# Performance work log

Hardware: AMD Instinct MI355X
Metric: run time of the kernel (lower is better)

Reference implementation:

```python
import jax, jax.numpy as jnp
import numpy as np

DIM = 1024
H = 16
D = DIM // H  # 64
M = 64
TAU = 0.1


def setup_inputs() -> dict:
    key = jax.random.key(0)
    ks = jax.random.split(key, 12)
    s = 1.0 / np.sqrt(DIM)
    inp = {
        "x": jax.random.normal(ks[0], (4, 2048, DIM), dtype=jnp.float32),
        "W_q": jax.random.uniform(ks[1], (DIM, DIM), jnp.float32, -s, s),
        "b_q": jax.random.uniform(ks[2], (DIM,), jnp.float32, -s, s),
        "W_k": jax.random.uniform(ks[3], (DIM, DIM), jnp.float32, -s, s),
        "b_k": jax.random.uniform(ks[4], (DIM,), jnp.float32, -s, s),
        "W_v": jax.random.uniform(ks[5], (DIM, DIM), jnp.float32, -s, s),
        "b_v": jax.random.uniform(ks[6], (DIM,), jnp.float32, -s, s),
        "W_alpha": jax.random.uniform(ks[7], (H * M, DIM), jnp.float32, -s, s),
        "b_alpha": jax.random.uniform(ks[8], (H * M,), jnp.float32, -s, s),
        "W_o": jax.random.uniform(ks[9], (DIM, DIM), jnp.float32, -s, s),
        "b_o": jax.random.uniform(ks[10], (DIM,), jnp.float32, -s, s),
    }
    return inp


def reference(x, W_q, b_q, W_k, b_k, W_v, b_v, W_alpha, b_alpha, W_o, b_o):
    B, S, _ = x.shape
    silu = jax.nn.silu
    # projections [B,S,H,D]
    q = silu(x @ W_q.T + b_q).reshape(B, S, H, D)
    k = silu(x @ W_k.T + b_k).reshape(B, S, H, D)
    v = silu(x @ W_v.T + b_v).reshape(B, S, H, D)
    alpha = jax.nn.sigmoid(x @ W_alpha.T + b_alpha) ** (1.0 / TAU)
    alpha = alpha.reshape(B, S, H, M)

    # time-major for scan: [S, B, H, ...]
    qT = jnp.moveaxis(q, 1, 0)
    kT = jnp.moveaxis(k, 1, 0)
    vT = jnp.moveaxis(v, 1, 0)
    aT = jnp.moveaxis(alpha, 1, 0)

    Ke0 = jnp.zeros((B, H, M, D), dtype=x.dtype)
    Ve0 = jnp.zeros((B, H, M, D), dtype=x.dtype)

    def step(carry, inputs):
        Ke, Ve = carry
        q_t, k_t, v_t, a_t = inputs  # [B,H,D], [B,H,D], [B,H,D], [B,H,M]
        a = a_t[..., None]  # [B,H,M,1]
        Ke = a * Ke + (1.0 - a) * k_t[:, :, None, :]
        Ve = a * Ve + (1.0 - a) * v_t[:, :, None, :]
        energy = jnp.einsum("bhmd,bhd->bhm", Ke, q_t)
        attn = jax.nn.softmax(energy, axis=-1)
        o_t = jnp.einsum("bhm,bhmd->bhd", attn, Ve)
        return (Ke, Ve), o_t

    _, oT = jax.lax.scan(step, (Ke0, Ve0), (qT, kT, vT, aT))  # [S,B,H,D]
    o = jnp.moveaxis(oT, 0, 1).reshape(B, S, H * D)
    return o @ W_o.T + b_o
```

## Files before the change

kernel.cpp:

```cpp
#include <hip/hip_runtime.h>

#define S_LEN 2048
#define KDIM 1024
#define EMIT 64
#define WARM 16

typedef __attribute__((ext_vector_type(4))) float f32x4;
typedef __attribute__((ext_vector_type(8))) _Float16 f16x8;
typedef __attribute__((ext_vector_type(4))) _Float16 f16x4;
typedef __attribute__((ext_vector_type(2))) _Float16 f16x2;

union U8 { f16x8 v; f16x2 p[4]; };

__device__ inline f16x2 bcast2(_Float16 x) { f16x2 r; r[0] = x; r[1] = x; return r; }

#if __has_builtin(__builtin_amdgcn_fdot2)
__device__ inline float fdot2(f16x2 a, f16x2 b, float c) { return __builtin_amdgcn_fdot2(a, b, c, false); }
#else
__device__ inline float fdot2(f16x2 a, f16x2 b, float c) {
    return c + (float)a[0] * (float)b[0] + (float)a[1] * (float)b[1];
}
#endif

__device__ inline void async16(const void* g, void* l) {
    typedef unsigned int __attribute__((address_space(1)))* gp_t;
    typedef unsigned int __attribute__((address_space(3)))* lp_t;
    __builtin_amdgcn_global_load_lds((gp_t)g, (lp_t)l, 16, 0, 0);
}

__global__ void cvt_f16(const float* __restrict__ s, _Float16* __restrict__ d, int n4) {
    int i = blockIdx.x * 256 + threadIdx.x;
    int st = gridDim.x * 256;
    for (; i < n4; i += st) {
        f32x4 v = ((const f32x4*)s)[i];
        f16x4 o;
        o[0] = (_Float16)v[0]; o[1] = (_Float16)v[1];
        o[2] = (_Float16)v[2]; o[3] = (_Float16)v[3];
        ((f16x4*)d)[i] = o;
    }
}

__global__ void cvt_w5(const float* __restrict__ w0, const float* __restrict__ w1,
                       const float* __restrict__ w2, const float* __restrict__ w3,
                       const float* __restrict__ w4,
                       _Float16* __restrict__ dcat, _Float16* __restrict__ dwo) {
    const int seg = blockIdx.y;
    const float* s = seg == 0 ? w0 : seg == 1 ? w1 : seg == 2 ? w2 : seg == 3 ? w3 : w4;
    _Float16* d = (seg < 4) ? (dcat + (size_t)seg * 1048576) : dwo;
    const int n4 = 1024 * 1024 / 4;
    int i = blockIdx.x * 256 + threadIdx.x;
    const int st = gridDim.x * 256;
    for (; i < n4; i += st) {
        f32x4 v = ((const f32x4*)s)[i];
        f16x4 o;
        o[0] = (_Float16)v[0]; o[1] = (_Float16)v[1];
        o[2] = (_Float16)v[2]; o[3] = (_Float16)v[3];
        ((f16x4*)d)[i] = o;
    }
}

template<int EPI>
__global__ __launch_bounds__(256)
void gemm_bt(const _Float16* __restrict__ A, const _Float16* __restrict__ Bw,
             const float* __restrict__ bias0, const float* __restrict__ bias1,
             const float* __restrict__ bias2, const float* __restrict__ bias3,
             _Float16* __restrict__ outS, float* __restrict__ outF)
{
    __shared__ _Float16 ldsA[128 * 32];
    __shared__ _Float16 ldsB[128 * 32];
    const int tid = threadIdx.x;
    const int l = tid & 63, wid = tid >> 6;
    const int bm = blockIdx.x, bn = blockIdx.y;
    const int wr = wid >> 1, wc = wid & 1;

    f32x4 acc[4][4];
#pragma unroll
    for (int i = 0; i < 4; i++)
#pragma unroll
        for (int j = 0; j < 4; j++) { f32x4 z = {0.f, 0.f, 0.f, 0.f}; acc[i][j] = z; }

    const int rsub = wid * 16 + (l >> 2);
    const int ck = (l & 3) * 8;
    const _Float16* ga = A + (size_t)(bm * 128 + rsub) * KDIM + ck;
    const _Float16* gb = Bw + (size_t)(bn * 128 + rsub) * KDIM + ck;
    char* la = (char*)ldsA + wid * 1024;
    char* lb = (char*)ldsB + wid * 1024;

    for (int kt = 0; kt < KDIM / 32; ++kt) {
        __syncthreads();
        const _Float16* gak = ga + kt * 32;
        const _Float16* gbk = gb + kt * 32;
        async16(gak, la);
        async16(gak + (size_t)64 * KDIM, la + 4096);
        async16(gbk, lb);
        async16(gbk + (size_t)64 * KDIM, lb + 4096);
        __syncthreads();

        f16x8 af[4], bfr[4];
        const int rowb = l & 15;
        const int kb = (l >> 4) * 16;
#pragma unroll
        for (int mi = 0; mi < 4; mi++)
            af[mi] = *(const f16x8*)((const char*)ldsA + (wr * 64 + mi * 16 + rowb) * 64 + kb);
#pragma unroll
        for (int ni = 0; ni < 4; ni++)
            bfr[ni] = *(const f16x8*)((const char*)ldsB + (wc * 64 + ni * 16 + rowb) * 64 + kb);
#pragma unroll
        for (int mi = 0; mi < 4; mi++)
#pragma unroll
            for (int ni = 0; ni < 4; ni++)
                acc[mi][ni] = __builtin_amdgcn_mfma_f32_16x16x32_f16(af[mi], bfr[ni], acc[mi][ni], 0, 0, 0);
    }

    if (EPI == 0) {
        const int proj = bn >> 3;
        const int colbase = (bn & 7) * 128;
        const float* bias = proj == 0 ? bias0 : proj == 1 ? bias1 : proj == 2 ? bias2 : bias3;
        const int part = proj == 0 ? 2 : proj == 1 ? 0 : proj == 2 ? 1 : 3;
#pragma unroll
        for (int mi = 0; mi < 4; mi++) {
#pragma unroll
            for (int ni = 0; ni < 4; ni++) {
                const int c = colbase + wc * 64 + ni * 16 + (l & 15);
                const int h = c >> 6, jj = c & 63;
                const float bv = bias[c];
#pragma unroll
                for (int i = 0; i < 4; i++) {
                    const int gr = bm * 128 + wr * 64 + mi * 16 + ((l >> 4) * 4 + i);
                    const int b = gr >> 11, t = gr & 2047;
                    float z = acc[mi][ni][i] + bv;
                    float sg = 1.f / (1.f + __expf(-z));
                    float val;
                    if (proj < 3) val = z * sg;
                    else { float p2 = sg * sg, p4 = p2 * p2, p8 = p4 * p4; val = p8 * p2; }
                    outS[(((size_t)(b * 16 + h) * S_LEN + t) * 4 + part) * 64 + jj] = (_Float16)val;
                }
            }
        }
    } else {
#pragma unroll
        for (int mi = 0; mi < 4; mi++)
#pragma unroll
            for (int ni = 0; ni < 4; ni++) {
                const int gc = bn * 128 + wc * 64 + ni * 16 + (l & 15);
                const float bv = bias0[gc];
#pragma unroll
                for (int i = 0; i < 4; i++) {
                    const int gr = bm * 128 + wr * 64 + mi * 16 + ((l >> 4) * 4 + i);
                    outF[(size_t)gr * 1024 + gc] = acc[mi][ni][i] + bv;
                }
            }
    }
}

__global__ __launch_bounds__(256)
void scan_fused(const _Float16* __restrict__ strm, _Float16* __restrict__ oh)
{
    __shared__ float eb[2][256];
    __shared__ float obuf[2][256];
    __shared__ _Float16 at16[64];
    const int tid = threadIdx.x, l = tid & 63, w = tid >> 6;
    const int bh = blockIdx.x, c = blockIdx.y;
    const int b = bh >> 4, h = bh & 15;
    const int warm = (c == 0) ? 0 : WARM;
    const int start = c * EMIT - warm;
    const int nsteps = warm + EMIT;
    const f16x2 one2 = bcast2((_Float16)1.f);

    f16x2 ke2[8], ve2[8];
#pragma unroll
    for (int j = 0; j < 8; ++j) { ke2[j] = bcast2((_Float16)0.f); ve2[j] = bcast2((_Float16)0.f); }

    const _Float16* rp = strm + (size_t)(bh * S_LEN + start) * 256;
    _Float16* op = oh + (size_t)b * S_LEN * 1024 + h * 64 + l;

    U8 kA, kB, aA, aB, qA, qB;
    kA.v = *(const f16x8*)(rp + w * 16);
    kB.v = *(const f16x8*)(rp + w * 16 + 8);
    aA.v = *(const f16x8*)(rp + 192 + w * 16);
    aB.v = *(const f16x8*)(rp + 192 + w * 16 + 8);
    _Float16 a_l = rp[192 + l];
    _Float16 v_l = rp[64 + l];

    for (int s = 0; s < warm; ++s) {
        const f16x2 am2 = bcast2(a_l);
        const f16x2 om2 = one2 - am2;
        const f16x2 vd2 = bcast2(v_l);
#pragma unroll
        for (int j = 0; j < 4; ++j) {
            ke2[j]     = am2 * ke2[j]     + om2 * kA.p[j];
            ke2[4 + j] = am2 * ke2[4 + j] + om2 * kB.p[j];
            ve2[j]     = aA.p[j] * (ve2[j]     - vd2) + vd2;
            ve2[4 + j] = aB.p[j] * (ve2[4 + j] - vd2) + vd2;
        }
        const _Float16* r2 = rp + (size_t)(s + 1) * 256;
        kA.v = *(const f16x8*)(r2 + w * 16);
        kB.v = *(const f16x8*)(r2 + w * 16 + 8);
        aA.v = *(const f16x8*)(r2 + 192 + w * 16);
        aB.v = *(const f16x8*)(r2 + 192 + w * 16 + 8);
        a_l = r2[192 + l];
        v_l = r2[64 + l];
    }

    {
        const _Float16* r2 = rp + (size_t)warm * 256;
        qA.v = *(const f16x8*)(r2 + 128 + w * 16);
        qB.v = *(const f16x8*)(r2 + 128 + w * 16 + 8);
    }

    for (int s = warm; s < nsteps; ++s) {
        const int ep = (s - warm) & 1;
        const f16x2 am2 = bcast2(a_l);
        const f16x2 om2 = one2 - am2;
        const f16x2 vd2 = bcast2(v_l);
        float e0 = 0.f, e1 = 0.f;
#pragma unroll
        for (int j = 0; j < 4; ++j) {
            ke2[j]     = am2 * ke2[j]     + om2 * kA.p[j];
            ke2[4 + j] = am2 * ke2[4 + j] + om2 * kB.p[j];
            e0 = fdot2(ke2[j],     qA.p[j], e0);
            e1 = fdot2(ke2[4 + j], qB.p[j], e1);
            ve2[j]     = aA.p[j] * (ve2[j]     - vd2) + vd2;
            ve2[4 + j] = aB.p[j] * (ve2[4 + j] - vd2) + vd2;
        }
        eb[ep][tid] = e0 + e1;
        __syncthreads();

        if (s + 1 < nsteps) {
            const _Float16* r2 = rp + (size_t)(s + 1) * 256;
            kA.v = *(const f16x8*)(r2 + w * 16);
            kB.v = *(const f16x8*)(r2 + w * 16 + 8);
            aA.v = *(const f16x8*)(r2 + 192 + w * 16);
            aB.v = *(const f16x8*)(r2 + 192 + w * 16 + 8);
            qA.v = *(const f16x8*)(r2 + 128 + w * 16);
            qB.v = *(const f16x8*)(r2 + 128 + w * 16 + 8);
            a_l = r2[192 + l];
            v_l = r2[64 + l];
        }
        if (w == 0 && s > warm) {
            const int q = 1 - ep;
            const float o4 = obuf[q][l] + obuf[q][64 + l] + obuf[q][128 + l] + obuf[q][192 + l];
            op[(size_t)(start + s - 1) * 1024] = (_Float16)o4;
        }
        const float E = eb[ep][l] + eb[ep][64 + l] + eb[ep][128 + l] + eb[ep][192 + l];
        const float pr = __expf(E);
        float ps = pr;
#pragma unroll
        for (int d2 = 1; d2 < 64; d2 <<= 1) ps += __shfl_xor(ps, d2);
        const float at = pr / ps;
        if ((l >> 4) == w) at16[l] = (_Float16)at;
        U8 A0, A1;
        A0.v = *(const f16x8*)&at16[w * 16];
        A1.v = *(const f16x8*)&at16[w * 16 + 8];
        float o0 = 0.f, o1 = 0.f;
#pragma unroll
        for (int j = 0; j < 4; ++j) {
            o0 = fdot2(A0.p[j], ve2[j],     o0);
            o1 = fdot2(A1.p[j], ve2[4 + j], o1);
        }
        obuf[ep][tid] = o0 + o1;
    }
    __syncthreads();
    if (w == 0) {
        const int ep = (EMIT - 1) & 1;
        const float o4 = obuf[ep][l] + obuf[ep][64 + l] + obuf[ep][128 + l] + obuf[ep][192 + l];
        op[(size_t)(start + nsteps - 1) * 1024] = (_Float16)o4;
    }
}

extern "C" void kernel_launch(void* const* d_in, const int* in_sizes, int n_in,
                              void* d_out, int out_size, void* d_ws, size_t ws_size,
                              hipStream_t stream)
{
    const float* x  = (const float*)d_in[0];
    const float* Wq = (const float*)d_in[1];
    const float* bq = (const float*)d_in[2];
    const float* Wk = (const float*)d_in[3];
    const float* bk = (const float*)d_in[4];
    const float* Wv = (const float*)d_in[5];
    const float* bv = (const float*)d_in[6];
    const float* Wa = (const float*)d_in[7];
    const float* ba = (const float*)d_in[8];
    const float* Wo = (const float*)d_in[9];
    const float* bo = (const float*)d_in[10];
    float* out = (float*)d_out;

    char* w = (char*)d_ws;
    _Float16* xh   = (_Float16*)(w);
    _Float16* wcat = (_Float16*)(w + (16ull << 20));
    _Float16* woh  = (_Float16*)(w + (24ull << 20));
    _Float16* strm = (_Float16*)(w + (26ull << 20));
    _Float16* oh   = (_Float16*)(w + (90ull << 20));

    cvt_f16<<<512, 256, 0, stream>>>(x, xh, 8192 * 1024 / 4);
    cvt_w5<<<dim3(256, 5), 256, 0, stream>>>(Wq, Wk, Wv, Wa, Wo, wcat, woh);

    gemm_bt<0><<<dim3(64, 32), 256, 0, stream>>>(xh, wcat, bq, bk, bv, ba, strm, nullptr);

    scan_fused<<<dim3(64, 32), 256, 0, stream>>>(strm, oh);

    gemm_bt<1><<<dim3(64, 8), 256, 0, stream>>>(oh, woh, bo, nullptr, nullptr, nullptr, nullptr, out);
}
```

Baseline: 370.6 us.

## Process two scan steps per barrier and remap GEMM block order for XCDs

The scan loop now advances two timesteps per iteration. It computes both energy vectors before a single __syncthreads, runs both softmaxes and output dots together, and stores the intermediate V state so step one's output uses the right value. This halves the per-step barrier and LDS round-trip latency on the serial recurrence, at the cost of more registers and double-buffered loads. The GEMM also remaps linear block ids so consecutive tiles land on the same XCD (stride of 8), which should improve L2 locality. The remap hardcodes bm = newid & 63, which assumes a grid of 64 row tiles.

```diff
diff --git a/kernel.cpp b/kernel.cpp
--- a/kernel.cpp
+++ b/kernel.cpp
@@ -70,7 +70,11 @@
     __shared__ _Float16 ldsB[128 * 32];
     const int tid = threadIdx.x;
     const int l = tid & 63, wid = tid >> 6;
-    const int bm = blockIdx.x, bn = blockIdx.y;
+    const int fid = blockIdx.x + ((int)gridDim.x) * blockIdx.y;
+    const int per = ((int)(gridDim.x * gridDim.y)) >> 3;
+    const int newid = (fid & 7) * per + (fid >> 3);
+    const int bm = newid & 63;
+    const int bn = newid >> 6;
     const int wr = wid >> 1, wc = wid & 1;
 
     f32x4 acc[4][4];
@@ -157,8 +161,8 @@
 void scan_fused(const _Float16* __restrict__ strm, _Float16* __restrict__ oh)
 {
     __shared__ float eb[2][256];
-    __shared__ float obuf[2][256];
-    __shared__ _Float16 at16[64];
+    __shared__ float obuf[2][2][256];
+    __shared__ _Float16 at16[2][64];
     const int tid = threadIdx.x, l = tid & 63, w = tid >> 6;
     const int bh = blockIdx.x, c = blockIdx.y;
     const int b = bh >> 4, h = bh & 15;
@@ -167,104 +171,168 @@
     const int nsteps = warm + EMIT;
     const f16x2 one2 = bcast2((_Float16)1.f);
 
-    f16x2 ke2[8], ve2[8];
+    f16x2 ke2[8], ve2[8], vsn[8];
 #pragma unroll
     for (int j = 0; j < 8; ++j) { ke2[j] = bcast2((_Float16)0.f); ve2[j] = bcast2((_Float16)0.f); }
 
     const _Float16* rp = strm + (size_t)(bh * S_LEN + start) * 256;
     _Float16* op = oh + (size_t)b * S_LEN * 1024 + h * 64 + l;
 
-    U8 kA, kB, aA, aB, qA, qB;
-    kA.v = *(const f16x8*)(rp + w * 16);
-    kB.v = *(const f16x8*)(rp + w * 16 + 8);
-    aA.v = *(const f16x8*)(rp + 192 + w * 16);
-    aB.v = *(const f16x8*)(rp + 192 + w * 16 + 8);
-    _Float16 a_l = rp[192 + l];
-    _Float16 v_l = rp[64 + l];
+    U8 kA0, kB0, aA0, aB0, qA0, qB0, kA1, kB1, aA1, aB1, qA1, qB1;
+    kA0.v = *(const f16x8*)(rp + w * 16);
+    kB0.v = *(const f16x8*)(rp + w * 16 + 8);
+    aA0.v = *(const f16x8*)(rp + 192 + w * 16);
+    aB0.v = *(const f16x8*)(rp + 192 + w * 16 + 8);
+    _Float16 a0 = rp[192 + l];
+    _Float16 v0 = rp[64 + l];
+    _Float16 a1, v1;
 
     for (int s = 0; s < warm; ++s) {
-        const f16x2 am2 = bcast2(a_l);
+        const f16x2 am2 = bcast2(a0);
         const f16x2 om2 = one2 - am2;
-        const f16x2 vd2 = bcast2(v_l);
+        const f16x2 vd2 = bcast2(v0);
 #pragma unroll
         for (int j = 0; j < 4; ++j) {
-            ke2[j]     = am2 * ke2[j]     + om2 * kA.p[j];
-            ke2[4 + j] = am2 * ke2[4 + j] + om2 * kB.p[j];
-            ve2[j]     = aA.p[j] * (ve2[j]     - vd2) + vd2;
-            ve2[4 + j] = aB.p[j] * (ve2[4 + j] - vd2) + vd2;
+            ke2[j]     = am2 * ke2[j]     + om2 * kA0.p[j];
+            ke2[4 + j] = am2 * ke2[4 + j] + om2 * kB0.p[j];
+            ve2[j]     = aA0.p[j] * (ve2[j]     - vd2) + vd2;
+            ve2[4 + j] = aB0.p[j] * (ve2[4 + j] - vd2) + vd2;
         }
         const _Float16* r2 = rp + (size_t)(s + 1) * 256;
-        kA.v = *(const f16x8*)(r2 + w * 16);
-        kB.v = *(const f16x8*)(r2 + w * 16 + 8);
-        aA.v = *(const f16x8*)(r2 + 192 + w * 16);
-        aB.v = *(const f16x8*)(r2 + 192 + w * 16 + 8);
-        a_l = r2[192 + l];
-        v_l = r2[64 + l];
+        kA0.v = *(const f16x8*)(r2 + w * 16);
+        kB0.v = *(const f16x8*)(r2 + w * 16 + 8);
+        aA0.v = *(const f16x8*)(r2 + 192 + w * 16);
+        aB0.v = *(const f16x8*)(r2 + 192 + w * 16 + 8);
+        a0 = r2[192 + l];
+        v0 = r2[64 + l];
     }
 
     {
-        const _Float16* r2 = rp + (size_t)warm * 256;
-        qA.v = *(const f16x8*)(r2 + 128 + w * 16);
-        qB.v = *(const f16x8*)(r2 + 128 + w * 16 + 8);
-    }
-
-    for (int s = warm; s < nsteps; ++s) {
-        const int ep = (s - warm) & 1;
-        const f16x2 am2 = bcast2(a_l);
-        const f16x2 om2 = one2 - am2;
-        const f16x2 vd2 = bcast2(v_l);
-        float e0 = 0.f, e1 = 0.f;
+        const _Float16* r0 = rp + (size_t)warm * 256;
+        qA0.v = *(const f16x8*)(r0 + 128 + w * 16);
+        qB0.v = *(const f16x8*)(r0 + 128 + w * 16 + 8);
+        const _Float16* r1 = r0 + 256;
+        kA1.v = *(const f16x8*)(r1 + w * 16);
+        kB1.v = *(const f16x8*)(r1 + w * 16 + 8);
+        qA1.v = *(const f16x8*)(r1 + 128 + w * 16);
+        qB1.v = *(const f16x8*)(r1 + 128 + w * 16 + 8);
+        aA1.v = *(const f16x8*)(r1 + 192 + w * 16);
+        aB1.v = *(const f16x8*)(r1 + 192 + w * 16 + 8);
+        a1 = r1[192 + l];
+        v1 = r1[64 + l];
+    }
+
+    for (int s = warm; s < nsteps; s += 2) {
+        const int pp = ((s - warm) >> 1) & 1;
+        {
+            const f16x2 am2 = bcast2(a0);
+            const f16x2 om2 = one2 - am2;
+            const f16x2 vd2 = bcast2(v0);
+            float e0 = 0.f, e1 = 0.f;
+#pragma unroll
+            for (int j = 0; j < 4; ++j) {
+                ke2[j]     = am2 * ke2[j]     + om2 * kA0.p[j];
+                ke2[4 + j] = am2 * ke2[4 + j] + om2 * kB0.p[j];
+                e0 = fdot2(ke2[j],     qA0.p[j], e0);
+                e1 = fdot2(ke2[4 + j], qB0.p[j], e1);
+                ve2[j]     = aA0.p[j] * (ve2[j]     - vd2) + vd2;
+                ve2[4 + j] = aB0.p[j] * (ve2[4 + j] - vd2) + vd2;
+            }
+#pragma unroll
+            for (int j = 0; j < 8; ++j) vsn[j] = ve2[j];
+            eb[0][tid] = e0 + e1;
+        }
+        {
+            const f16x2 am2 = bcast2(a1);
+            const f16x2 om2 = one2 - am2;
+            const f16x2 vd2 = bcast2(v1);
+            float e0 = 0.f, e1 = 0.f;
+#pragma unroll
+            for (int j = 0; j < 4; ++j) {
+                ke2[j]     = am2 * ke2[j]     + om2 * kA1.p[j];
+                ke2[4 + j] = am2 * ke2[4 + j] + om2 * kB1.p[j];
+                e0 = fdot2(ke2[j],     qA1.p[j], e0);
+                e1 = fdot2(ke2[4 + j], qB1.p[j], e1);
+                ve2[j]     = aA1.p[j] * (ve2[j]     - vd2) + vd2;
+                ve2[4 + j] = aB1.p[j] * (ve2[4 + j] - vd2) + vd2;
+            }
+            eb[1][tid] = e0 + e1;
+        }
+        __syncthreads();
+
+        if (s + 2 < nsteps) {
+            const _Float16* r0 = rp + (size_t)(s + 2) * 256;
+            kA0.v = *(const f16x8*)(r0 + w * 16);
+            kB0.v = *(const f16x8*)(r0 + w * 16 + 8);
+            qA0.v = *(const f16x8*)(r0 + 128 + w * 16);
+            qB0.v = *(const f16x8*)(r0 + 128 + w * 16 + 8);
+            aA0.v = *(const f16x8*)(r0 + 192 + w * 16);
+            aB0.v = *(const f16x8*)(r0 + 192 + w * 16 + 8);
+            a0 = r0[192 + l];
+            v0 = r0[64 + l];
+            const _Float16* r1 = r0 + 256;
+            kA1.v = *(const f16x8*)(r1 + w * 16);
+            kB1.v = *(const f16x8*)(r1 + w * 16 + 8);
+            qA1.v = *(const f16x8*)(r1 + 128 + w * 16);
+            qB1.v = *(const f16x8*)(r1 + 128 + w * 16 + 8);
+            aA1.v = *(const f16x8*)(r1 + 192 + w * 16);
+            aB1.v = *(const f16x8*)(r1 + 192 + w * 16 + 8);
+            a1 = r1[192 + l];
+            v1 = r1[64 + l];
+        }
+        if (s > warm) {
+            const int qq = 1 - pp;
+            if (w == 0) {
+                const float o4 = obuf[qq][0][l] + obuf[qq][0][64 + l] +
+                                 obuf[qq][0][128 + l] + obuf[qq][0][192 + l];
+                op[(size_t)(start + s - 2) * 1024] = (_Float16)o4;
+            } else if (w == 1) {
+                const float o4 = obuf[qq][1][l] + obuf[qq][1][64 + l] +
+                                 obuf[qq][1][128 + l] + obuf[qq][1][192 + l];
+                op[(size_t)(start + s - 1) * 1024] = (_Float16)o4;
+            }
+        }
+        const float E0 = eb[0][l] + eb[0][64 + l] + eb[0][128 + l] + eb[0][192 + l];
+        const float E1 = eb[1][l] + eb[1][64 + l] + eb[1][128 + l] + eb[1][192 + l];
+        const float p0 = __expf(E0);
+        const float p1 = __expf(E1);
+        float s0 = p0, s1 = p1;
+#pragma unroll
+        for (int d2 = 1; d2 < 64; d2 <<= 1) {
+            s0 += __shfl_xor(s0, d2);
+            s1 += __shfl_xor(s1, d2);
+        }
+        const float at0 = p0 / s0;
+        const float at1 = p1 / s1;
+        if ((l >> 4) == w) { at16[0][l] = (_Float16)at0; at16[1][l] = (_Float16)at1; }
+        U8 A0, A1, B0, B1;
+        A0.v = *(const f16x8*)&at16[0][w * 16];
+        A1.v = *(const f16x8*)&at16[0][w * 16 + 8];
+        B0.v = *(const f16x8*)&at16[1][w * 16];
+        B1.v = *(const f16x8*)&at16[1][w * 16 + 8];
+        float o00 = 0.f, o01 = 0.f, o10 = 0.f, o11 = 0.f;
 #pragma unroll
         for (int j = 0; j < 4; ++j) {
-            ke2[j]     = am2 * ke2[j]     + om2 * kA.p[j];
-            ke2[4 + j] = am2 * ke2[4 + j] + om2 * kB.p[j];
-            e0 = fdot2(ke2[j],     qA.p[j], e0);
-            e1 = fdot2(ke2[4 + j], qB.p[j], e1);
-            ve2[j]     = aA.p[j] * (ve2[j]     - vd2) + vd2;
-            ve2[4 + j] = aB.p[j] * (ve2[4 + j] - vd2) + vd2;
-        }
-        eb[ep][tid] = e0 + e1;
-        __syncthreads();
-
-        if (s + 1 < nsteps) {
-            const _Float16* r2 = rp + (size_t)(s + 1) * 256;
-            kA.v = *(const f16x8*)(r2 + w * 16);
-            kB.v = *(const f16x8*)(r2 + w * 16 + 8);
-            aA.v = *(const f16x8*)(r2 + 192 + w * 16);
-            aB.v = *(const f16x8*)(r2 + 192 + w * 16 + 8);
-            qA.v = *(const f16x8*)(r2 + 128 + w * 16);
-            qB.v = *(const f16x8*)(r2 + 128 + w * 16 + 8);
-            a_l = r2[192 + l];
-            v_l = r2[64 + l];
-        }
-        if (w == 0 && s > warm) {
-            const int q = 1 - ep;
-            const float o4 = obuf[q][l] + obuf[q][64 + l] + obuf[q][128 + l] + obuf[q][192 + l];
-            op[(size_t)(start + s - 1) * 1024] = (_Float16)o4;
-        }
-        const float E = eb[ep][l] + eb[ep][64 + l] + eb[ep][128 + l] + eb[ep][192 + l];
-        const float pr = __expf(E);
-        float ps = pr;
-#pragma unroll
-        for (int d2 = 1; d2 < 64; d2 <<= 1) ps += __shfl_xor(ps, d2);
-        const float at = pr / ps;
-        if ((l >> 4) == w) at16[l] = (_Float16)at;
-        U8 A0, A1;
-        A0.v = *(const f16x8*)&at16[w * 16];
-        A1.v = *(const f16x8*)&at16[w * 16 + 8];
-        float o0 = 0.f, o1 = 0.f;
-#pragma unroll
-        for (int j = 0; j < 4; ++j) {
-            o0 = fdot2(A0.p[j], ve2[j],     o0);
-            o1 = fdot2(A1.p[j], ve2[4 + j], o1);
-        }
-        obuf[ep][tid] = o0 + o1;
+            o00 = fdot2(A0.p[j], vsn[j],     o00);
+            o01 = fdot2(A1.p[j], vsn[4 + j], o01);
+            o10 = fdot2(B0.p[j], ve2[j],     o10);
+            o11 = fdot2(B1.p[j], ve2[4 + j], o11);
+        }
+        obuf[pp][0][tid] = o00 + o01;
+        obuf[pp][1][tid] = o10 + o11;
     }
     __syncthreads();
-    if (w == 0) {
-        const int ep = (EMIT - 1) & 1;
-        const float o4 = obuf[ep][l] + obuf[ep][64 + l] + obuf[ep][128 + l] + obuf[ep][192 + l];
-        op[(size_t)(start + nsteps - 1) * 1024] = (_Float16)o4;
+    {
+        const int pp = ((EMIT - 2) >> 1) & 1;
+        if (w == 0) {
+            const float o4 = obuf[pp][0][l] + obuf[pp][0][64 + l] +
+                             obuf[pp][0][128 + l] + obuf[pp][0][192 + l];
+            op[(size_t)(start + nsteps - 2) * 1024] = (_Float16)o4;
+        } else if (w == 1) {
+            const float o4 = obuf[pp][1][l] + obuf[pp][1][64 + l] +
+                             obuf[pp][1][128 + l] + obuf[pp][1][192 + l];
+            op[(size_t)(start + nsteps - 1) * 1024] = (_Float16)o4;
+        }
     }
 }
 
```

Result: slower. 388.1 us (+4.7%).
